# Optimization experiments

Measured on AMD Instinct MI355X. Metric: run time of the kernel, lower is better.

Reference implementation:

```python
import jax, jax.numpy as jnp
import numpy as np

C_IN = 768
CA = 384


def dwconv3d(x, w, b, pad):
    # x: [B, Ca, T, H, W], w: [Ca, 1, kd, kh, kw] depthwise (groups=Ca)
    y = jax.lax.conv_general_dilated(
        x, w, window_strides=(1, 1, 1), padding=pad,
        dimension_numbers=("NCDHW", "OIDHW", "NCDHW"),
        feature_group_count=w.shape[0])
    return y + b[None, :, None, None, None]


def setup_inputs() -> dict:
    key = jax.random.key(0)
    ks = jax.random.split(key, 9)
    s = 0.02
    inp = {
        "x": jax.random.normal(ks[0], (128, 197, C_IN), dtype=jnp.float32),
        # main branch params (torch Linear weight transposed to [in, out])
        "w1": jax.random.normal(ks[1], (C_IN, CA), dtype=jnp.float32) * s,
        "b1": jnp.zeros((CA,), jnp.float32),
        "cw": jax.random.normal(ks[2], (CA, 1, 3, 3, 3), dtype=jnp.float32) * s,
        "cb": jnp.zeros((CA,), jnp.float32),
        "w2": jax.random.normal(ks[3], (CA, C_IN), dtype=jnp.float32) * s,
        "b2": jnp.zeros((C_IN,), jnp.float32),
        # offset-adapter params (depthwise kernel (1,3,3))
        "ow1": jax.random.normal(ks[4], (C_IN, CA), dtype=jnp.float32) * s,
        "ob1": jnp.zeros((CA,), jnp.float32),
        "ocw": jax.random.normal(ks[5], (CA, 1, 1, 3, 3), dtype=jnp.float32) * s,
        "ocb": jnp.zeros((CA,), jnp.float32),
        "ow2": jax.random.normal(ks[6], (CA, C_IN), dtype=jnp.float32) * s,
        "ob2": jnp.zeros((C_IN,), jnp.float32),
        "T": 8,
    }
    return inp


def reference(x, w1, b1, cw, cb, w2, b2, ow1, ob1, ocw, ocb, ow2, ob2, T):
    BT, L, C = x.shape
    B = BT // T
    H = W = int(round((L - 1) ** 0.5))
    Ca = w1.shape[1]

    xs = x[:, 1:, :].reshape(B, T, H * W, C)  # drop CLS token

    # ---- OffsetAdapter branch ----
    x_former = jnp.concatenate([xs[:, :1], xs[:, :-1]], axis=1)  # former_id = [0,0,1,...,T-2]
    off = xs - x_former
    off = off @ ow1 + ob1                                   # [B,T,HW,Ca]
    off = off.reshape(B, T, H, W, Ca).transpose(0, 4, 1, 2, 3)  # [B,Ca,T,H,W]
    off = dwconv3d(off, ocw, ocb, [(0, 0), (1, 1), (1, 1)])
    off = off.transpose(0, 2, 3, 4, 1).reshape(BT, H * W, Ca)
    off = off @ ow2 + ob2                                   # [BT,HW,C]

    # ---- main branch ----
    y = xs @ w1 + b1                                        # [B,T,HW,Ca]
    y = y.reshape(B, T, H, W, Ca).transpose(0, 4, 1, 2, 3)  # [B,Ca,T,H,W]
    y = dwconv3d(y, cw, cb, [(1, 1), (1, 1), (1, 1)])
    y = y.transpose(0, 2, 3, 4, 1).reshape(BT, H * W, Ca)
    y = y @ w2 + b2 + off                                   # [BT,HW,C]

    # residual add into patch tokens (CLS passthrough)
    return x.at[:, 1:, :].add(y)
```

## Files before the change

kernel.cpp:

```cpp
#include <hip/hip_runtime.h>

#define Cc   768
#define CAc  384
#define Tc   8
#define Hc   14
#define Wc   14
#define HWc  196
#define Lc   197
#define BTc  128
#define Mc   25088

typedef unsigned short u16;
typedef __attribute__((ext_vector_type(4))) float f32x4;
typedef __attribute__((ext_vector_type(4))) short s16x4;
typedef __attribute__((ext_vector_type(8))) short s16x8;

__device__ __forceinline__ u16 f2b(float f) {
  union { float f; unsigned u; } v; v.f = f;
  unsigned r = (v.u + 0x7FFFu + ((v.u >> 16) & 1u)) >> 16;
  return (u16)r;
}
__device__ __forceinline__ float b2f(u16 h) {
  union { unsigned u; float f; } v; v.u = ((unsigned)h) << 16;
  return v.f;
}

__global__ void wt_kernel(const float* __restrict__ wA, u16* __restrict__ wAT,
                          const float* __restrict__ wB, u16* __restrict__ wBT,
                          int K, int N) {
  __shared__ float t[32][33];
  const float* w = blockIdx.z ? wB : wA;
  u16* wT = blockIdx.z ? wBT : wAT;
  int k0 = blockIdx.x * 32, n0 = blockIdx.y * 32;
  int tx = threadIdx.x & 31, ty = threadIdx.x >> 5;
  #pragma unroll
  for (int p = 0; p < 4; ++p) {
    int r = ty + p * 8;
    t[r][tx] = w[(long)(k0 + r) * N + n0 + tx];
  }
  __syncthreads();
  #pragma unroll
  for (int p = 0; p < 4; ++p) {
    int r = ty + p * 8;
    wT[(long)(n0 + r) * K + k0 + tx] = f2b(t[tx][r]);
  }
}

__global__ void cwt_kernel(const float* __restrict__ cw, float* __restrict__ cwT, int taps) {
  int idx = blockIdx.x * 256 + threadIdx.x;
  if (idx >= taps * CAc) return;
  int t = idx / CAc, c = idx - t * CAc;
  cwT[idx] = cw[c * taps + t];
}

__global__ void prep_kernel(const float* __restrict__ x, u16* __restrict__ xb, u16* __restrict__ db) {
  int idx = blockIdx.x * 256 + threadIdx.x;
  int c8 = idx % 96;
  int rest = idx / 96;
  int hw = rest % HWc;
  int b = rest / HWc;
  int c0 = c8 * 8;
  f32x4 pa, pb;
  #pragma unroll
  for (int t = 0; t < Tc; ++t) {
    long xoff = ((long)(b * Tc + t) * Lc + 1 + hw) * Cc + c0;
    f32x4 ca = *(const f32x4*)(x + xoff);
    f32x4 cb = *(const f32x4*)(x + xoff + 4);
    if (t == 0) { pa = ca; pb = cb; }
    s16x8 xo, dd;
    #pragma unroll
    for (int q = 0; q < 4; ++q) {
      xo[q]     = (short)f2b(ca[q]);
      xo[q + 4] = (short)f2b(cb[q]);
      dd[q]     = (short)f2b(ca[q] - pa[q]);
      dd[q + 4] = (short)f2b(cb[q] - pb[q]);
    }
    long r = (long)(b * Tc + t) * HWc + hw;
    *(s16x8*)(xb + r * Cc + c0) = xo;
    *(s16x8*)(db + r * Cc + c0) = dd;
    pa = ca; pb = cb;
  }
}

__global__ void cls_kernel(const float* __restrict__ x, float* __restrict__ out) {
  int idx = blockIdx.x * 256 + threadIdx.x;
  if (idx >= BTc * (Cc / 4)) return;
  int bt = idx / (Cc / 4);
  int c4 = (idx - bt * (Cc / 4)) * 4;
  long o = (long)bt * Lc * Cc + c4;
  *(f32x4*)(out + o) = *(const f32x4*)(x + o);
}

#define SP 72

__global__ __launch_bounds__(256, 4) void gemm1_kernel(
    const u16* __restrict__ xb, const u16* __restrict__ db,
    const u16* __restrict__ w1T, const u16* __restrict__ ow1T,
    const float* __restrict__ b1v, const float* __restrict__ ob1v,
    u16* __restrict__ y1, u16* __restrict__ o1)
{
  __shared__ u16 lA[128 * SP];
  __shared__ u16 lB[128 * SP];
  const u16* A    = blockIdx.z ? db   : xb;
  const u16* Wt   = blockIdx.z ? ow1T : w1T;
  const float* bv = blockIdx.z ? ob1v : b1v;
  u16* outp       = blockIdx.z ? o1   : y1;

  int tid = threadIdx.x;
  int m0 = blockIdx.x * 128;
  int n0 = blockIdx.y * 128;
  int wave = tid >> 6, lane = tid & 63;
  int wm = (wave >> 1) * 64, wn = (wave & 1) * 64;
  int lrow = lane & 15, lgrp = lane >> 4;
  int srow = tid >> 3;
  int scol = (tid & 7) * 8;

  f32x4 acc[4][4];
  #pragma unroll
  for (int i = 0; i < 4; ++i)
    #pragma unroll
    for (int j = 0; j < 4; ++j) acc[i][j] = (f32x4){0,0,0,0};

  for (int kt = 0; kt < 12; ++kt) {
    int k0 = kt * 64;
    #pragma unroll
    for (int p = 0; p < 4; ++p) {
      int r = p * 32 + srow;
      s16x8 va = *(const s16x8*)(A  + (long)(m0 + r) * Cc + k0 + scol);
      s16x8 vb = *(const s16x8*)(Wt + (long)(n0 + r) * Cc + k0 + scol);
      *(s16x8*)(lA + r * SP + scol) = va;
      *(s16x8*)(lB + r * SP + scol) = vb;
    }
    __syncthreads();
    #pragma unroll
    for (int kk = 0; kk < 2; ++kk) {
      s16x8 af[4], bf[4];
      #pragma unroll
      for (int i = 0; i < 4; ++i) af[i] = *(const s16x8*)(lA + (wm + i * 16 + lrow) * SP + kk * 32 + lgrp * 8);
      #pragma unroll
      for (int j = 0; j < 4; ++j) bf[j] = *(const s16x8*)(lB + (wn + j * 16 + lrow) * SP + kk * 32 + lgrp * 8);
      #pragma unroll
      for (int i = 0; i < 4; ++i)
        #pragma unroll
        for (int j = 0; j < 4; ++j)
          acc[i][j] = __builtin_amdgcn_mfma_f32_16x16x32_bf16(af[i], bf[j], acc[i][j], 0, 0, 0);
    }
    __syncthreads();
  }
  #pragma unroll
  for (int i = 0; i < 4; ++i) {
    #pragma unroll
    for (int j = 0; j < 4; ++j) {
      int n = n0 + wn + j * 16 + lrow;
      float bb = bv[n];
      #pragma unroll
      for (int q = 0; q < 4; ++q) {
        int m = m0 + wm + i * 16 + lgrp * 4 + q;
        outp[(long)m * CAc + n] = f2b(acc[i][j][q] + bb);
      }
    }
  }
}

__global__ __launch_bounds__(256, 4) void gemm2_kernel(
    const u16* __restrict__ c1, const u16* __restrict__ c2,
    const u16* __restrict__ w2T, const u16* __restrict__ ow2T,
    const float* __restrict__ b2v, const float* __restrict__ ob2v,
    const float* __restrict__ x, float* __restrict__ out)
{
  __shared__ u16 lA[128 * SP];
  __shared__ u16 lB[128 * SP];
  int tid = threadIdx.x;
  int m0 = blockIdx.x * 128;
  int n0 = blockIdx.y * 128;
  int wave = tid >> 6, lane = tid & 63;
  int wm = (wave >> 1) * 64, wn = (wave & 1) * 64;
  int lrow = lane & 15, lgrp = lane >> 4;
  int srow = tid >> 3;
  int scol = (tid & 7) * 8;

  f32x4 acc[4][4];
  #pragma unroll
  for (int i = 0; i < 4; ++i)
    #pragma unroll
    for (int j = 0; j < 4; ++j) acc[i][j] = (f32x4){0,0,0,0};

  for (int kt = 0; kt < 12; ++kt) {
    int half = kt >= 6;
    const u16* Ap = half ? c2 : c1;
    const u16* Wp = half ? ow2T : w2T;
    int k0 = (half ? (kt - 6) : kt) * 64;
    #pragma unroll
    for (int p = 0; p < 4; ++p) {
      int r = p * 32 + srow;
      s16x8 va = *(const s16x8*)(Ap + (long)(m0 + r) * CAc + k0 + scol);
      s16x8 vb = *(const s16x8*)(Wp + (long)(n0 + r) * CAc + k0 + scol);
      *(s16x8*)(lA + r * SP + scol) = va;
      *(s16x8*)(lB + r * SP + scol) = vb;
    }
    __syncthreads();
    #pragma unroll
    for (int kk = 0; kk < 2; ++kk) {
      s16x8 af[4], bf[4];
      #pragma unroll
      for (int i = 0; i < 4; ++i) af[i] = *(const s16x8*)(lA + (wm + i * 16 + lrow) * SP + kk * 32 + lgrp * 8);
      #pragma unroll
      for (int j = 0; j < 4; ++j) bf[j] = *(const s16x8*)(lB + (wn + j * 16 + lrow) * SP + kk * 32 + lgrp * 8);
      #pragma unroll
      for (int i = 0; i < 4; ++i)
        #pragma unroll
        for (int j = 0; j < 4; ++j)
          acc[i][j] = __builtin_amdgcn_mfma_f32_16x16x32_bf16(af[i], bf[j], acc[i][j], 0, 0, 0);
    }
    __syncthreads();
  }
  #pragma unroll
  for (int i = 0; i < 4; ++i) {
    #pragma unroll
    for (int q = 0; q < 4; ++q) {
      int m = m0 + wm + i * 16 + lgrp * 4 + q;
      int bt = m / HWc;
      int hw = m - bt * HWc;
      long base = ((long)bt * Lc + 1 + hw) * Cc;
      #pragma unroll
      for (int j = 0; j < 4; ++j) {
        int n = n0 + wn + j * 16 + lrow;
        out[base + n] = x[base + n] + acc[i][j][q] + b2v[n] + ob2v[n];
      }
    }
  }
}

__global__ void conv_kernel(const u16* __restrict__ in1, const float* __restrict__ wT1,
                            const float* __restrict__ bias1, u16* __restrict__ out1,
                            const u16* __restrict__ in2, const float* __restrict__ wT2,
                            const float* __restrict__ bias2, u16* __restrict__ out2)
{
  int bid = blockIdx.x;
  int swz = (bid & 7) * 448 + (bid >> 3);
  int is3d = swz < 1792;
  int bth = is3d ? swz : swz - 1792;

  const u16* in = is3d ? in1 : in2;
  const float* wT = is3d ? wT1 : wT2;
  const float* bias = is3d ? bias1 : bias2;
  u16* outp = is3d ? out1 : out2;

  int h = bth % Hc;
  int bt = bth / Hc;
  int t = bt % Tc;
  int tid = threadIdx.x;
  int dtlo = is3d ? -1 : 0, dthi = is3d ? 1 : 0;
  for (int it = tid; it < Wc * 48; it += 256) {
    int wq = it / 48;
    int c = (it - wq * 48) * 8;
    float a[8] = {0,0,0,0,0,0,0,0};
    int tap = 0;
    for (int dt = dtlo; dt <= dthi; ++dt) {
      int tt = t + dt;
      bool tok = (tt >= 0) && (tt < Tc);
      for (int dh = -1; dh <= 1; ++dh) {
        int hh = h + dh;
        bool hok = (hh >= 0) && (hh < Hc);
        for (int dw = -1; dw <= 1; ++dw, ++tap) {
          int ww = wq + dw;
          if (!tok || !hok || ww < 0 || ww >= Wc) continue;
          const u16* ip = in + ((long)(bt + dt) * HWc + hh * Wc + ww) * CAc + c;
          s16x8 v = *(const s16x8*)ip;
          const float* wp = wT + tap * CAc + c;
          f32x4 w0 = *(const f32x4*)wp;
          f32x4 w1 = *(const f32x4*)(wp + 4);
          #pragma unroll
          for (int q = 0; q < 4; ++q) {
            a[q]     += b2f((u16)v[q])     * w0[q];
            a[q + 4] += b2f((u16)v[q + 4]) * w1[q];
          }
        }
      }
    }
    s16x8 o;
    #pragma unroll
    for (int q = 0; q < 8; ++q) o[q] = (short)f2b(a[q] + bias[c + q]);
    *(s16x8*)(outp + ((long)bt * HWc + h * Wc + wq) * CAc + c) = o;
  }
}

extern "C" void kernel_launch(void* const* d_in, const int* in_sizes, int n_in,
                              void* d_out, int out_size, void* d_ws, size_t ws_size,
                              hipStream_t stream) {
  const float* x   = (const float*)d_in[0];
  const float* w1  = (const float*)d_in[1];
  const float* b1  = (const float*)d_in[2];
  const float* cw  = (const float*)d_in[3];
  const float* cb  = (const float*)d_in[4];
  const float* w2  = (const float*)d_in[5];
  const float* b2  = (const float*)d_in[6];
  const float* ow1 = (const float*)d_in[7];
  const float* ob1 = (const float*)d_in[8];
  const float* ocw = (const float*)d_in[9];
  const float* ocb = (const float*)d_in[10];
  const float* ow2 = (const float*)d_in[11];
  const float* ob2 = (const float*)d_in[12];
  float* out = (float*)d_out;
  char* ws = (char*)d_ws;

  u16*  w1T  = (u16*) (ws + 0);
  u16*  ow1T = (u16*) (ws + 589824);
  u16*  w2T  = (u16*) (ws + 1179648);
  u16*  ow2T = (u16*) (ws + 1769472);
  float* cwT = (float*)(ws + 2359296);
  float* ocwT= (float*)(ws + 2400768);
  u16*  xb   = (u16*) (ws + 2414592);
  u16*  db   = (u16*) (ws + 40949760);
  u16*  y1   = (u16*) (ws + 79484928);
  u16*  o1   = (u16*) (ws + 98752512);
  u16*  c1   = (u16*) (ws + 2414592);
  u16*  c2   = (u16*) (ws + 21682176);

  wt_kernel<<<dim3(24, 12, 2), 256, 0, stream>>>(w1, w1T, ow1, ow1T, 768, 384);
  wt_kernel<<<dim3(12, 24, 2), 256, 0, stream>>>(w2, w2T, ow2, ow2T, 384, 768);
  cwt_kernel<<<41, 256, 0, stream>>>(cw, cwT, 27);
  cwt_kernel<<<14, 256, 0, stream>>>(ocw, ocwT, 9);
  cls_kernel<<<96, 256, 0, stream>>>(x, out);
  prep_kernel<<<1176, 256, 0, stream>>>(x, xb, db);
  gemm1_kernel<<<dim3(196, 3, 2), 256, 0, stream>>>(xb, db, w1T, ow1T, b1, ob1, y1, o1);
  conv_kernel<<<3584, 256, 0, stream>>>(y1, cwT, cb, c1, o1, ocwT, ocb, c2);
  gemm2_kernel<<<dim3(196, 6), 256, 0, stream>>>(c1, c2, w2T, ow2T, b2, ob2, x, out);
}
```

Baseline: 375.0 us.

## Reuse input columns across W in depthwise conv and swizzle GEMM block order

The depthwise conv kernel is restructured so each thread keeps seven output columns for four channels in registers. Each loaded input row is reused across the three W taps, which cuts redundant global loads and weight loads per output. Both GEMM kernels switch to a 1D grid with an XCD-aware swizzle so that all N-tiles of the same M-tile are scheduled together, aiming for better L2 reuse of the A rows. The risks are higher register pressure from the 28 accumulators and a changed block-to-XCD mapping.

```diff
diff --git a/kernel.cpp b/kernel.cpp
--- a/kernel.cpp
+++ b/kernel.cpp
@@ -101,14 +101,18 @@
 {
   __shared__ u16 lA[128 * SP];
   __shared__ u16 lB[128 * SP];
-  const u16* A    = blockIdx.z ? db   : xb;
-  const u16* Wt   = blockIdx.z ? ow1T : w1T;
-  const float* bv = blockIdx.z ? ob1v : b1v;
-  u16* outp       = blockIdx.z ? o1   : y1;
+  int bid = blockIdx.x;
+  int swz = (bid & 7) * 147 + (bid >> 3);
+  int mt = swz / 6, r6 = swz % 6;
+  int zb = r6 / 3, nt = r6 % 3;
+  const u16* A    = zb ? db   : xb;
+  const u16* Wt   = zb ? ow1T : w1T;
+  const float* bv = zb ? ob1v : b1v;
+  u16* outp       = zb ? o1   : y1;
 
   int tid = threadIdx.x;
-  int m0 = blockIdx.x * 128;
-  int n0 = blockIdx.y * 128;
+  int m0 = mt * 128;
+  int n0 = nt * 128;
   int wave = tid >> 6, lane = tid & 63;
   int wm = (wave >> 1) * 64, wn = (wave & 1) * 64;
   int lrow = lane & 15, lgrp = lane >> 4;
@@ -170,9 +174,12 @@
 {
   __shared__ u16 lA[128 * SP];
   __shared__ u16 lB[128 * SP];
+  int bid = blockIdx.x;
+  int swz = (bid & 7) * 147 + (bid >> 3);
+  int mt = swz / 6, nt = swz % 6;
   int tid = threadIdx.x;
-  int m0 = blockIdx.x * 128;
-  int n0 = blockIdx.y * 128;
+  int m0 = mt * 128;
+  int n0 = nt * 128;
   int wave = tid >> 6, lane = tid & 63;
   int wm = (wave >> 1) * 64, wn = (wave & 1) * 64;
   int lrow = lane & 15, lgrp = lane >> 4;
@@ -231,57 +238,75 @@
   }
 }
 
-__global__ void conv_kernel(const u16* __restrict__ in1, const float* __restrict__ wT1,
-                            const float* __restrict__ bias1, u16* __restrict__ out1,
-                            const u16* __restrict__ in2, const float* __restrict__ wT2,
-                            const float* __restrict__ bias2, u16* __restrict__ out2)
+__global__ __launch_bounds__(192) void conv_kernel(
+    const u16* __restrict__ in1, const float* __restrict__ wT1,
+    const float* __restrict__ bias1, u16* __restrict__ out1,
+    const u16* __restrict__ in2, const float* __restrict__ wT2,
+    const float* __restrict__ bias2, u16* __restrict__ out2)
 {
-  int bid = blockIdx.x;
-  int swz = (bid & 7) * 448 + (bid >> 3);
-  int is3d = swz < 1792;
-  int bth = is3d ? swz : swz - 1792;
-
+  int bx = blockIdx.x;
+  int swzx = (bx & 7) * 224 + (bx >> 3);
+  int is3d = (blockIdx.y == 0);
   const u16* in = is3d ? in1 : in2;
   const float* wT = is3d ? wT1 : wT2;
   const float* bias = is3d ? bias1 : bias2;
   u16* outp = is3d ? out1 : out2;
 
-  int h = bth % Hc;
-  int bt = bth / Hc;
-  int t = bt % Tc;
+  int h = swzx % Hc;
+  int bt = swzx / Hc;
+  int t = bt & 7;
   int tid = threadIdx.x;
+  int c4 = tid % 96;
+  int wh = tid / 96;
+  int c0 = c4 * 4;
+  int wstart = wh * 7;
+
+  float acc[7][4];
+  #pragma unroll
+  for (int j = 0; j < 7; ++j)
+    #pragma unroll
+    for (int q = 0; q < 4; ++q) acc[j][q] = 0.f;
+
   int dtlo = is3d ? -1 : 0, dthi = is3d ? 1 : 0;
-  for (int it = tid; it < Wc * 48; it += 256) {
-    int wq = it / 48;
-    int c = (it - wq * 48) * 8;
-    float a[8] = {0,0,0,0,0,0,0,0};
-    int tap = 0;
-    for (int dt = dtlo; dt <= dthi; ++dt) {
-      int tt = t + dt;
-      bool tok = (tt >= 0) && (tt < Tc);
-      for (int dh = -1; dh <= 1; ++dh) {
-        int hh = h + dh;
-        bool hok = (hh >= 0) && (hh < Hc);
-        for (int dw = -1; dw <= 1; ++dw, ++tap) {
-          int ww = wq + dw;
-          if (!tok || !hok || ww < 0 || ww >= Wc) continue;
-          const u16* ip = in + ((long)(bt + dt) * HWc + hh * Wc + ww) * CAc + c;
-          s16x8 v = *(const s16x8*)ip;
-          const float* wp = wT + tap * CAc + c;
-          f32x4 w0 = *(const f32x4*)wp;
-          f32x4 w1 = *(const f32x4*)(wp + 4);
-          #pragma unroll
-          for (int q = 0; q < 4; ++q) {
-            a[q]     += b2f((u16)v[q])     * w0[q];
-            a[q + 4] += b2f((u16)v[q + 4]) * w1[q];
-          }
+  for (int dt = dtlo; dt <= dthi; ++dt) {
+    int tt = t + dt;
+    if (tt < 0 || tt >= Tc) continue;
+    for (int dh = -1; dh <= 1; ++dh) {
+      int hh = h + dh;
+      if (hh < 0 || hh >= Hc) continue;
+      int tapbase = is3d ? ((dt + 1) * 9 + (dh + 1) * 3) : ((dh + 1) * 3);
+      f32x4 k0 = *(const f32x4*)(wT + (tapbase + 0) * CAc + c0);
+      f32x4 k1 = *(const f32x4*)(wT + (tapbase + 1) * CAc + c0);
+      f32x4 k2 = *(const f32x4*)(wT + (tapbase + 2) * CAc + c0);
+      long rowbase = ((long)(bt + dt) * HWc + hh * Wc) * CAc + c0;
+      #pragma unroll
+      for (int i = 0; i < 9; ++i) {
+        int col = wstart - 1 + i;
+        if (col < 0 || col >= Wc) continue;
+        s16x4 v = *(const s16x4*)(in + rowbase + (long)col * CAc);
+        f32x4 f;
+        #pragma unroll
+        for (int q = 0; q < 4; ++q) f[q] = b2f((u16)v[q]);
+        if (i <= 6) {
+          for (int q = 0; q < 4; ++q) acc[i][q]     += f[q] * k0[q];
+        }
+        if (i >= 1 && i <= 7) {
+          for (int q = 0; q < 4; ++q) acc[i - 1][q] += f[q] * k1[q];
+        }
+        if (i >= 2) {
+          for (int q = 0; q < 4; ++q) acc[i - 2][q] += f[q] * k2[q];
         }
       }
     }
-    s16x8 o;
-    #pragma unroll
-    for (int q = 0; q < 8; ++q) o[q] = (short)f2b(a[q] + bias[c + q]);
-    *(s16x8*)(outp + ((long)bt * HWc + h * Wc + wq) * CAc + c) = o;
+  }
+  f32x4 bv = *(const f32x4*)(bias + c0);
+  long obase = ((long)bt * HWc + h * Wc + wstart) * CAc + c0;
+  #pragma unroll
+  for (int j = 0; j < 7; ++j) {
+    s16x4 o;
+    #pragma unroll
+    for (int q = 0; q < 4; ++q) o[q] = (short)f2b(acc[j][q] + bv[q]);
+    *(s16x4*)(outp + obase + (long)j * CAc) = o;
   }
 }
 
@@ -323,7 +348,7 @@
   cwt_kernel<<<14, 256, 0, stream>>>(ocw, ocwT, 9);
   cls_kernel<<<96, 256, 0, stream>>>(x, out);
   prep_kernel<<<1176, 256, 0, stream>>>(x, xb, db);
-  gemm1_kernel<<<dim3(196, 3, 2), 256, 0, stream>>>(xb, db, w1T, ow1T, b1, ob1, y1, o1);
-  conv_kernel<<<3584, 256, 0, stream>>>(y1, cwT, cb, c1, o1, ocwT, ocb, c2);
-  gemm2_kernel<<<dim3(196, 6), 256, 0, stream>>>(c1, c2, w2T, ow2T, b2, ob2, x, out);
-}
+  gemm1_kernel<<<1176, 256, 0, stream>>>(xb, db, w1T, ow1T, b1, ob1, y1, o1);
+  conv_kernel<<<dim3(1792, 2), 192, 0, stream>>>(y1, cwT, cb, c1, o1, ocwT, ocb, c2);
+  gemm2_kernel<<<1176, 256, 0, stream>>>(c1, c2, w2T, ow2T, b2, ob2, x, out);
+}
```

New measurement: 315.7 us. 1.19x faster.
